# Kernel optimization log

Hardware: AMD Instinct MI355X
Metric: run time of the kernel (lower is better)

Reference implementation:

```python
import jax, jax.numpy as jnp
import numpy as np

B, T, F, H, C = 512, 512, 128, 32, 6

def setup_inputs() -> dict:
    key = jax.random.key(0)
    ks = jax.random.split(key, 6)
    x = jax.random.normal(ks[0], (B, T, F), jnp.float32)
    # random valid lengths; zero-padded tails get masked by Masking(mask_value=0.0)
    lengths = jax.random.randint(ks[1], (B,), T // 4, T + 1)
    tmask = (jnp.arange(T)[None, :] < lengths[:, None]).astype(jnp.float32)
    x = x * tmask[:, :, None]
    Wx = jax.random.normal(ks[2], (F, 4 * H), jnp.float32) / np.sqrt(F).astype(np.float32)
    Wh = jax.random.normal(ks[3], (H, 4 * H), jnp.float32) / np.sqrt(H).astype(np.float32)
    b = jnp.zeros((4 * H,), jnp.float32)
    Wfc = jax.random.normal(ks[4], (H, C), jnp.float32) / np.sqrt(H).astype(np.float32)
    bfc = jnp.zeros((C,), jnp.float32)
    return dict(x=x, Wx=Wx, Wh=Wh, b=b, Wfc=Wfc, bfc=bfc)

def reference(x, Wx, Wh, b, Wfc, bfc):
    # Masking(0.0): timestep masked iff all features == 0
    mask = jnp.any(x != 0.0, axis=-1)                       # [B, T]
    Hh = Wh.shape[0]
    Bn = x.shape[0]
    xt = jnp.transpose(x, (1, 0, 2))                        # [T, B, F]
    mt = jnp.transpose(mask, (1, 0))[:, :, None].astype(x.dtype)  # [T, B, 1]
    # precompute input projection for all steps (one big GEMM)
    xz = jnp.einsum('tbf,fk->tbk', xt, Wx) + b              # [T, B, 4H]

    def step(carry, inp):
        h, c = carry
        zx, m = inp
        z = zx + h @ Wh                                     # [B, 4H]
        i, f, g, o = jnp.split(z, 4, axis=-1)               # keras gate order i,f,c,o
        i = jax.nn.sigmoid(i)
        f = jax.nn.sigmoid(f)
        g = jnp.tanh(g)
        o = jax.nn.sigmoid(o)
        c_new = f * c + i * g
        h_new = o * jnp.tanh(c_new)
        # masked steps keep previous state (Keras masked LSTM semantics)
        h = m * h_new + (1.0 - m) * h
        c = m * c_new + (1.0 - m) * c
        return (h, c), None

    h0 = jnp.zeros((Bn, Hh), x.dtype)
    (h, _), _ = jax.lax.scan(step, (h0, h0), (xz, mt))
    return jax.nn.softmax(h @ Wfc + bfc, axis=-1)           # [B, C]
```

## Files before the change

kernel.cpp:

```cpp
#include <hip/hip_runtime.h>

#define B_ 512
#define T_ 512
#define F_ 128
#define H_ 32
#define C_ 6

__global__ __launch_bounds__(256, 2) void k_xz(
    const float* __restrict__ x, const float* __restrict__ W,
    const float* __restrict__ bias, float* __restrict__ xz,
    float* __restrict__ mask)
{
  __shared__ float xl[128 * 64];
  __shared__ float wl[64 * 128];
  const int tid = threadIdx.x;
  const int m0  = blockIdx.x * 128;
  const int cg  = tid & 15;
  const int rg  = tid >> 4;

  float4 xpre[8], wpre[8];
  int rowbits = 0;

  auto load_chunk = [&](int ch) {
#pragma unroll
    for (int k = 0; k < 8; ++k) {
      const int u = tid + k * 256, r = u >> 4, q = u & 15;
      xpre[k] = *(const float4*)(x + (size_t)(m0 + r) * 128 + ch * 64 + q * 4);
    }
#pragma unroll
    for (int k = 0; k < 8; ++k) {
      const int u = tid + k * 256, f = u >> 5, q = u & 31;
      wpre[k] = *(const float4*)(W + (size_t)(ch * 64 + f) * 128 + q * 4);
    }
  };
  auto mask_chunk = [&]() {
#pragma unroll
    for (int k = 0; k < 8; ++k) {
      const float4 v = xpre[k];
      int nb = ((v.x != 0.f) || (v.y != 0.f) || (v.z != 0.f) || (v.w != 0.f)) ? 1 : 0;
      nb |= __shfl_xor(nb, 1); nb |= __shfl_xor(nb, 2);
      nb |= __shfl_xor(nb, 4); nb |= __shfl_xor(nb, 8);
      rowbits |= nb << k;
    }
  };
  auto write_chunk = [&]() {
#pragma unroll
    for (int k = 0; k < 8; ++k) {
      const int u = tid + k * 256, r = u >> 4, q = u & 15;
      *(float4*)(xl + r * 64 + ((q * 4) ^ (((r >> 3) & 3) << 2))) = xpre[k];
    }
#pragma unroll
    for (int k = 0; k < 8; ++k) {
      const int u = tid + k * 256, f = u >> 5, q = u & 31;
      *(float4*)(wl + f * 128 + q * 4) = wpre[k];
    }
  };

  float acc[8][8];
#pragma unroll
  for (int r = 0; r < 8; ++r)
#pragma unroll
    for (int u = 0; u < 8; ++u) acc[r][u] = 0.f;

  auto compute = [&]() {
#pragma unroll 2
    for (int fq = 0; fq < 16; ++fq) {
      float4 xv[8];
#pragma unroll
      for (int r = 0; r < 8; ++r)
        xv[r] = *(const float4*)(xl + (rg * 8 + r) * 64 + ((fq * 4) ^ ((rg & 3) << 2)));
#pragma unroll
      for (int ff = 0; ff < 4; ++ff) {
        const float* wr = wl + (fq * 4 + ff) * 128 + cg * 4;
        const float4 wa = *(const float4*)(wr);
        const float4 wb = *(const float4*)(wr + 64);
#pragma unroll
        for (int r = 0; r < 8; ++r) {
          const float xs = (ff == 0) ? xv[r].x : (ff == 1) ? xv[r].y
                         : (ff == 2) ? xv[r].z : xv[r].w;
          acc[r][0] += xs * wa.x;  acc[r][1] += xs * wa.y;
          acc[r][2] += xs * wa.z;  acc[r][3] += xs * wa.w;
          acc[r][4] += xs * wb.x;  acc[r][5] += xs * wb.y;
          acc[r][6] += xs * wb.z;  acc[r][7] += xs * wb.w;
        }
      }
    }
  };

  load_chunk(0);
  mask_chunk();
  write_chunk();
  __syncthreads();
  load_chunk(1);
  compute();
  __syncthreads();
  mask_chunk();
  write_chunk();
  __syncthreads();
  compute();

  float bb[8];
#pragma unroll
  for (int u = 0; u < 4; ++u) {
    bb[u]     = bias[cg * 4 + u];
    bb[4 + u] = bias[64 + cg * 4 + u];
  }
#pragma unroll
  for (int r = 0; r < 8; ++r) {
    float* op = xz + (size_t)(m0 + rg * 8 + r) * 128;
    float4 o0 = { acc[r][0] + bb[0], acc[r][1] + bb[1], acc[r][2] + bb[2], acc[r][3] + bb[3] };
    float4 o1 = { acc[r][4] + bb[4], acc[r][5] + bb[5], acc[r][6] + bb[6], acc[r][7] + bb[7] };
    *(float4*)(op + cg * 4)      = o0;
    *(float4*)(op + 64 + cg * 4) = o1;
  }
  if ((tid & 15) == 0) {
#pragma unroll
    for (int k = 0; k < 8; ++k)
      mask[m0 + k * 16 + rg] = (rowbits >> k) & 1 ? 1.f : 0.f;
  }
}

__device__ __forceinline__ float sigmf(float xx) {
  return __builtin_amdgcn_rcpf(1.f + __expf(-xx));
}
__device__ __forceinline__ float tanhf_(float xx) {
  return __builtin_amdgcn_rcpf(1.f + __expf(-2.f * xx)) * 2.f - 1.f;
}

__global__ __launch_bounds__(64, 1) void k_lstm(
    const float* __restrict__ xz, const float* __restrict__ mask,
    const float* __restrict__ Wh, const float* __restrict__ Wfc,
    const float* __restrict__ bfc, float* __restrict__ out)
{
  const int lane = threadIdx.x;
  const int half = lane >> 5;
  const int j    = lane & 31;
  const int b    = blockIdx.x;

  const int colA = half * 32 + j;
  const int colB = 64 + half * 32 + j;

  float WhA[32], WhB[32];
#pragma unroll
  for (int f = 0; f < 32; ++f) {
    WhA[f] = Wh[f * 128 + colA];
    WhB[f] = Wh[f * 128 + colB];
  }

  float hsc[32];
#pragma unroll
  for (int f = 0; f < 32; ++f) hsc[f] = 0.f;

  float cj = 0.f, hj = 0.f;

  const float* xrow = xz + (size_t)b * (T_ * 128);
  const float* mp   = mask + (size_t)b * T_;

  float xa[4], xb[4], mr[4];
#pragma unroll
  for (int s = 0; s < 4; ++s) {
    xa[s] = xrow[s * 128 + colA];
    xb[s] = xrow[s * 128 + colB];
    mr[s] = mp[s];
  }

  for (int t0 = 0; t0 < T_; t0 += 4) {
#pragma unroll
    for (int s = 0; s < 4; ++s) {
      const int t = t0 + s;
      float zA0 = xa[s], zA1 = 0.f;
      float zB0 = xb[s], zB1 = 0.f;
      const float m = mr[s];

      int pf = t + 4;
      if (pf > T_ - 1) pf = T_ - 1;
      xa[s] = xrow[(size_t)pf * 128 + colA];
      xb[s] = xrow[(size_t)pf * 128 + colB];
      mr[s] = mp[pf];

#pragma unroll
      for (int f = 0; f < 16; ++f) {
        zA0 += hsc[2 * f]     * WhA[2 * f];
        zA1 += hsc[2 * f + 1] * WhA[2 * f + 1];
        zB0 += hsc[2 * f]     * WhB[2 * f];
        zB1 += hsc[2 * f + 1] * WhB[2 * f + 1];
      }
      const float zA = zA0 + zA1;
      const float zB = zB0 + zB1;
      const float oA = __shfl_xor(zA, 32);
      const float oB = __shfl_xor(zB, 32);
      const float zi = half ? oA : zA;
      const float zf = half ? zA : oA;
      const float zg = half ? oB : zB;
      const float zo = half ? zB : oB;

      const float ig = sigmf(zi);
      const float fg = sigmf(zf);
      const float gg = tanhf_(zg);
      const float og = sigmf(zo);
      const float cn = fg * cj + ig * gg;
      const float hn = og * tanhf_(cn);
      cj += m * (cn - cj);
      hj += m * (hn - hj);

#pragma unroll
      for (int f = 0; f < 32; ++f)
        hsc[f] = __uint_as_float(__builtin_amdgcn_readlane(__float_as_uint(hj), f));
    }
  }

  float logits[C_];
#pragma unroll
  for (int c = 0; c < C_; ++c) {
    float aa = bfc[c];
#pragma unroll
    for (int f = 0; f < 32; ++f) aa += hsc[f] * Wfc[f * C_ + c];
    logits[c] = aa;
  }
  if (lane == 0) {
    float mx = logits[0];
#pragma unroll
    for (int c = 1; c < C_; ++c) mx = fmaxf(mx, logits[c]);
    float e[C_], sden = 0.f;
#pragma unroll
    for (int c = 0; c < C_; ++c) { e[c] = __expf(logits[c] - mx); sden += e[c]; }
    const float rs = 1.f / sden;
#pragma unroll
    for (int c = 0; c < C_; ++c) out[(size_t)b * C_ + c] = e[c] * rs;
  }
}

extern "C" void kernel_launch(void* const* d_in, const int* in_sizes, int n_in,
                              void* d_out, int out_size, void* d_ws, size_t ws_size,
                              hipStream_t stream) {
  const float* x   = (const float*)d_in[0];
  const float* Wx  = (const float*)d_in[1];
  const float* Wh  = (const float*)d_in[2];
  const float* bv  = (const float*)d_in[3];
  const float* Wfc = (const float*)d_in[4];
  const float* bfc = (const float*)d_in[5];
  float* out = (float*)d_out;

  float* xz   = (float*)d_ws;
  float* mask = (float*)((char*)d_ws + (size_t)B_ * T_ * 128 * 4);

  k_xz<<<(B_ * T_) / 128, 256, 0, stream>>>(x, Wx, bv, xz, mask);
  k_lstm<<<B_, 64, 0, stream>>>(xz, mask, Wh, Wfc, bfc, out);
}
```

Baseline: 271.3 us.

## Fuse input projection into LSTM kernel with producer-consumer warp specialization

Replaces the separate input-projection GEMM kernel and recurrent kernel with one fused kernel. Per block, four producer waves compute the x@Wx projection chunk by chunk into a double-buffered shared-memory ring, and two consumer waves run the recurrence for two batch rows. This removes the round trip of the large xz intermediate through global memory and one launch. In exchange the projection runs as a per-timestep dot product with 128-register weights instead of a tiled GEMM, every chunk adds a block-wide barrier, and each block carries a large shared-memory footprint.

```diff
diff --git a/kernel.cpp b/kernel.cpp
--- a/kernel.cpp
+++ b/kernel.cpp
@@ -5,120 +5,9 @@
 #define F_ 128
 #define H_ 32
 #define C_ 6
-
-__global__ __launch_bounds__(256, 2) void k_xz(
-    const float* __restrict__ x, const float* __restrict__ W,
-    const float* __restrict__ bias, float* __restrict__ xz,
-    float* __restrict__ mask)
-{
-  __shared__ float xl[128 * 64];
-  __shared__ float wl[64 * 128];
-  const int tid = threadIdx.x;
-  const int m0  = blockIdx.x * 128;
-  const int cg  = tid & 15;
-  const int rg  = tid >> 4;
-
-  float4 xpre[8], wpre[8];
-  int rowbits = 0;
-
-  auto load_chunk = [&](int ch) {
-#pragma unroll
-    for (int k = 0; k < 8; ++k) {
-      const int u = tid + k * 256, r = u >> 4, q = u & 15;
-      xpre[k] = *(const float4*)(x + (size_t)(m0 + r) * 128 + ch * 64 + q * 4);
-    }
-#pragma unroll
-    for (int k = 0; k < 8; ++k) {
-      const int u = tid + k * 256, f = u >> 5, q = u & 31;
-      wpre[k] = *(const float4*)(W + (size_t)(ch * 64 + f) * 128 + q * 4);
-    }
-  };
-  auto mask_chunk = [&]() {
-#pragma unroll
-    for (int k = 0; k < 8; ++k) {
-      const float4 v = xpre[k];
-      int nb = ((v.x != 0.f) || (v.y != 0.f) || (v.z != 0.f) || (v.w != 0.f)) ? 1 : 0;
-      nb |= __shfl_xor(nb, 1); nb |= __shfl_xor(nb, 2);
-      nb |= __shfl_xor(nb, 4); nb |= __shfl_xor(nb, 8);
-      rowbits |= nb << k;
-    }
-  };
-  auto write_chunk = [&]() {
-#pragma unroll
-    for (int k = 0; k < 8; ++k) {
-      const int u = tid + k * 256, r = u >> 4, q = u & 15;
-      *(float4*)(xl + r * 64 + ((q * 4) ^ (((r >> 3) & 3) << 2))) = xpre[k];
-    }
-#pragma unroll
-    for (int k = 0; k < 8; ++k) {
-      const int u = tid + k * 256, f = u >> 5, q = u & 31;
-      *(float4*)(wl + f * 128 + q * 4) = wpre[k];
-    }
-  };
-
-  float acc[8][8];
-#pragma unroll
-  for (int r = 0; r < 8; ++r)
-#pragma unroll
-    for (int u = 0; u < 8; ++u) acc[r][u] = 0.f;
-
-  auto compute = [&]() {
-#pragma unroll 2
-    for (int fq = 0; fq < 16; ++fq) {
-      float4 xv[8];
-#pragma unroll
-      for (int r = 0; r < 8; ++r)
-        xv[r] = *(const float4*)(xl + (rg * 8 + r) * 64 + ((fq * 4) ^ ((rg & 3) << 2)));
-#pragma unroll
-      for (int ff = 0; ff < 4; ++ff) {
-        const float* wr = wl + (fq * 4 + ff) * 128 + cg * 4;
-        const float4 wa = *(const float4*)(wr);
-        const float4 wb = *(const float4*)(wr + 64);
-#pragma unroll
-        for (int r = 0; r < 8; ++r) {
-          const float xs = (ff == 0) ? xv[r].x : (ff == 1) ? xv[r].y
-                         : (ff == 2) ? xv[r].z : xv[r].w;
-          acc[r][0] += xs * wa.x;  acc[r][1] += xs * wa.y;
-          acc[r][2] += xs * wa.z;  acc[r][3] += xs * wa.w;
-          acc[r][4] += xs * wb.x;  acc[r][5] += xs * wb.y;
-          acc[r][6] += xs * wb.z;  acc[r][7] += xs * wb.w;
-        }
-      }
-    }
-  };
-
-  load_chunk(0);
-  mask_chunk();
-  write_chunk();
-  __syncthreads();
-  load_chunk(1);
-  compute();
-  __syncthreads();
-  mask_chunk();
-  write_chunk();
-  __syncthreads();
-  compute();
-
-  float bb[8];
-#pragma unroll
-  for (int u = 0; u < 4; ++u) {
-    bb[u]     = bias[cg * 4 + u];
-    bb[4 + u] = bias[64 + cg * 4 + u];
-  }
-#pragma unroll
-  for (int r = 0; r < 8; ++r) {
-    float* op = xz + (size_t)(m0 + rg * 8 + r) * 128;
-    float4 o0 = { acc[r][0] + bb[0], acc[r][1] + bb[1], acc[r][2] + bb[2], acc[r][3] + bb[3] };
-    float4 o1 = { acc[r][4] + bb[4], acc[r][5] + bb[5], acc[r][6] + bb[6], acc[r][7] + bb[7] };
-    *(float4*)(op + cg * 4)      = o0;
-    *(float4*)(op + 64 + cg * 4) = o1;
-  }
-  if ((tid & 15) == 0) {
-#pragma unroll
-    for (int k = 0; k < 8; ++k)
-      mask[m0 + k * 16 + rg] = (rowbits >> k) & 1 ? 1.f : 0.f;
-  }
-}
+#define CH 32
+#define NCH (T_ / CH)
+
 
 __device__ __forceinline__ float sigmf(float xx) {
   return __builtin_amdgcn_rcpf(1.f + __expf(-xx));
@@ -127,16 +16,89 @@
   return __builtin_amdgcn_rcpf(1.f + __expf(-2.f * xx)) * 2.f - 1.f;
 }
 
-__global__ __launch_bounds__(64, 1) void k_lstm(
-    const float* __restrict__ xz, const float* __restrict__ mask,
-    const float* __restrict__ Wh, const float* __restrict__ Wfc,
-    const float* __restrict__ bfc, float* __restrict__ out)
+__global__ __launch_bounds__(384, 2) void k_fused(
+    const float* __restrict__ x, const float* __restrict__ Wx,
+    const float* __restrict__ bias, const float* __restrict__ Wh,
+    const float* __restrict__ Wfc, const float* __restrict__ bfc,
+    float* __restrict__ out)
 {
-  const int lane = threadIdx.x;
+  __shared__ float zring[2][2][CH][128];
+  __shared__ float xst  [2][2][CH][128];
+  __shared__ float mring[2][NCH][CH];
+
+  const int tid  = threadIdx.x;
+  const int wid  = tid >> 6;
+  const int lane = tid & 63;
+  const int brow = blockIdx.x * 2;
+
+  if (wid >= 2) {
+    const int p    = wid - 2;
+    const int prow = p >> 1;
+    const int hp   = p & 1;
+    const int cb   = hp * 64;
+    const int sb   = hp * 16;
+    const int r    = brow + prow;
+
+    float Wc[128];
+#pragma unroll
+    for (int f = 0; f < 128; ++f) Wc[f] = Wx[f * 128 + cb + lane];
+    const float bb = bias[cb + lane];
+    const float* xr = x + (size_t)r * (T_ * F_);
+
+    float2 xld[16];
+#pragma unroll
+    for (int s = 0; s < 16; ++s)
+      xld[s] = *(const float2*)(xr + (sb + s) * F_ + 2 * lane);
+#pragma unroll
+    for (int s = 0; s < 16; ++s) {
+      *(float2*)(&xst[prow][0][sb + s][2 * lane]) = xld[s];
+      const bool nb = (xld[s].x != 0.f) || (xld[s].y != 0.f);
+      const unsigned long long bal = __ballot(nb);
+      if (lane == 0) mring[prow][0][sb + s] = bal ? 1.f : 0.f;
+    }
+
+    for (int ph = 0; ph <= NCH; ++ph) {
+      __syncthreads();
+      if (ph >= NCH) continue;
+      const int slot = ph & 1;
+
+      if (ph + 1 < NCH) {
+#pragma unroll
+        for (int s = 0; s < 16; ++s)
+          xld[s] = *(const float2*)(xr + ((ph + 1) * CH + sb + s) * F_ + 2 * lane);
+      }
+
+      for (int t = 0; t < CH; ++t) {
+        float z0 = bb, z1 = 0.f, z2 = 0.f, z3 = 0.f;
+        const float* xp = &xst[prow][slot][t][0];
+#pragma unroll
+        for (int fq = 0; fq < 32; ++fq) {
+          const float4 xf = *(const float4*)(xp + fq * 4);
+          z0 += xf.x * Wc[fq * 4 + 0];
+          z1 += xf.y * Wc[fq * 4 + 1];
+          z2 += xf.z * Wc[fq * 4 + 2];
+          z3 += xf.w * Wc[fq * 4 + 3];
+        }
+        zring[prow][slot][t][cb + lane] = (z0 + z1) + (z2 + z3);
+      }
+
+      if (ph + 1 < NCH) {
+#pragma unroll
+        for (int s = 0; s < 16; ++s) {
+          *(float2*)(&xst[prow][slot ^ 1][sb + s][2 * lane]) = xld[s];
+          const bool nb = (xld[s].x != 0.f) || (xld[s].y != 0.f);
+          const unsigned long long bal = __ballot(nb);
+          if (lane == 0) mring[prow][ph + 1][sb + s] = bal ? 1.f : 0.f;
+        }
+      }
+    }
+    return;
+  }
+
+  const int row  = wid;
+  const int r    = brow + row;
   const int half = lane >> 5;
   const int j    = lane & 31;
-  const int b    = blockIdx.x;
-
   const int colA = half * 32 + j;
   const int colB = 64 + half * 32 + j;
 
@@ -150,62 +112,64 @@
   float hsc[32];
 #pragma unroll
   for (int f = 0; f < 32; ++f) hsc[f] = 0.f;
-
   float cj = 0.f, hj = 0.f;
 
-  const float* xrow = xz + (size_t)b * (T_ * 128);
-  const float* mp   = mask + (size_t)b * T_;
-
-  float xa[4], xb[4], mr[4];
-#pragma unroll
-  for (int s = 0; s < 4; ++s) {
-    xa[s] = xrow[s * 128 + colA];
-    xb[s] = xrow[s * 128 + colB];
-    mr[s] = mp[s];
-  }
-
-  for (int t0 = 0; t0 < T_; t0 += 4) {
-#pragma unroll
-    for (int s = 0; s < 4; ++s) {
-      const int t = t0 + s;
-      float zA0 = xa[s], zA1 = 0.f;
-      float zB0 = xb[s], zB1 = 0.f;
-      const float m = mr[s];
-
-      int pf = t + 4;
-      if (pf > T_ - 1) pf = T_ - 1;
-      xa[s] = xrow[(size_t)pf * 128 + colA];
-      xb[s] = xrow[(size_t)pf * 128 + colB];
-      mr[s] = mp[pf];
-
-#pragma unroll
-      for (int f = 0; f < 16; ++f) {
-        zA0 += hsc[2 * f]     * WhA[2 * f];
-        zA1 += hsc[2 * f + 1] * WhA[2 * f + 1];
-        zB0 += hsc[2 * f]     * WhB[2 * f];
-        zB1 += hsc[2 * f + 1] * WhB[2 * f + 1];
-      }
-      const float zA = zA0 + zA1;
-      const float zB = zB0 + zB1;
-      const float oA = __shfl_xor(zA, 32);
-      const float oB = __shfl_xor(zB, 32);
-      const float zi = half ? oA : zA;
-      const float zf = half ? zA : oA;
-      const float zg = half ? oB : zB;
-      const float zo = half ? zB : oB;
-
-      const float ig = sigmf(zi);
-      const float fg = sigmf(zf);
-      const float gg = tanhf_(zg);
-      const float og = sigmf(zo);
-      const float cn = fg * cj + ig * gg;
-      const float hn = og * tanhf_(cn);
-      cj += m * (cn - cj);
-      hj += m * (hn - hj);
-
-#pragma unroll
-      for (int f = 0; f < 32; ++f)
-        hsc[f] = __uint_as_float(__builtin_amdgcn_readlane(__float_as_uint(hj), f));
+  for (int ph = 0; ph <= NCH; ++ph) {
+    __syncthreads();
+    if (ph < 1) continue;
+    const int c    = ph - 1;
+    const int slot = c & 1;
+    const float* zb = &zring[row][slot][0][0];
+    const float* mb = &mring[row][c][0];
+
+    float za[4], zc[4], mm[4];
+#pragma unroll
+    for (int u = 0; u < 4; ++u) {
+      za[u] = zb[u * 128 + colA];
+      zc[u] = zb[u * 128 + colB];
+      mm[u] = mb[u];
+    }
+    for (int s0 = 0; s0 < 8; ++s0) {
+#pragma unroll
+      for (int u = 0; u < 4; ++u) {
+        const int s = s0 * 4 + u;
+        float zA0 = za[u], zA1 = 0.f;
+        float zB0 = zc[u], zB1 = 0.f;
+        const float m = mm[u];
+        if (s0 < 7) {
+          za[u] = zb[(s + 4) * 128 + colA];
+          zc[u] = zb[(s + 4) * 128 + colB];
+          mm[u] = mb[s + 4];
+        }
+#pragma unroll
+        for (int f = 0; f < 16; ++f) {
+          zA0 += hsc[2 * f]     * WhA[2 * f];
+          zA1 += hsc[2 * f + 1] * WhA[2 * f + 1];
+          zB0 += hsc[2 * f]     * WhB[2 * f];
+          zB1 += hsc[2 * f + 1] * WhB[2 * f + 1];
+        }
+        const float zA = zA0 + zA1;
+        const float zB = zB0 + zB1;
+        const float oA = __shfl_xor(zA, 32);
+        const float oB = __shfl_xor(zB, 32);
+        const float zi = half ? oA : zA;
+        const float zf = half ? zA : oA;
+        const float zg = half ? oB : zB;
+        const float zo = half ? zB : oB;
+
+        const float ig = sigmf(zi);
+        const float fg = sigmf(zf);
+        const float gg = tanhf_(zg);
+        const float og = sigmf(zo);
+        const float cn = fg * cj + ig * gg;
+        const float hn = og * tanhf_(cn);
+        cj += m * (cn - cj);
+        hj += m * (hn - hj);
+
+#pragma unroll
+        for (int f = 0; f < 32; ++f)
+          hsc[f] = __uint_as_float(__builtin_amdgcn_readlane(__float_as_uint(hj), f));
+      }
     }
   }
 
@@ -226,7 +190,7 @@
     for (int c = 0; c < C_; ++c) { e[c] = __expf(logits[c] - mx); sden += e[c]; }
     const float rs = 1.f / sden;
 #pragma unroll
-    for (int c = 0; c < C_; ++c) out[(size_t)b * C_ + c] = e[c] * rs;
+    for (int c = 0; c < C_; ++c) out[(size_t)r * C_ + c] = e[c] * rs;
   }
 }
 
@@ -241,9 +205,5 @@
   const float* bfc = (const float*)d_in[5];
   float* out = (float*)d_out;
 
-  float* xz   = (float*)d_ws;
-  float* mask = (float*)((char*)d_ws + (size_t)B_ * T_ * 128 * 4);
-
-  k_xz<<<(B_ * T_) / 128, 256, 0, stream>>>(x, Wx, bv, xz, mask);
-  k_lstm<<<B_, 64, 0, stream>>>(xz, mask, Wh, Wfc, bfc, out);
-}
+  k_fused<<<B_ / 2, 384, 0, stream>>>(x, Wx, bv, Wh, Wfc, bfc, out);
+}
```

Result: slower. 904.7 us (+233.5%).

## Stage LSTM input projections through double-buffered LDS chunks in recurrent kernel

Applied to the files above, without the earlier changes.

The recurrent kernel now copies each 32-step chunk of the precomputed input projection from global memory into a double-buffered shared-memory tile. The next chunk is loaded with coalesced float4 reads spread across the inner steps, and the mask row is preloaded into LDS. This replaces per-step scattered global loads with LDS reads, aiming to take global latency off the serial dependency chain. The dot product is also split into four accumulators per gate to shorten the FMA chain, and the launch-bounds occupancy hint is dropped. The cost is higher register pressure from the float4 staging registers and about 33 KB of shared memory per block.

```diff
diff --git a/kernel.cpp b/kernel.cpp
--- a/kernel.cpp
+++ b/kernel.cpp
@@ -5,6 +5,8 @@
 #define F_ 128
 #define H_ 32
 #define C_ 6
+#define CH 32
+#define NCH (T_ / CH)
 
 __global__ __launch_bounds__(256, 2) void k_xz(
     const float* __restrict__ x, const float* __restrict__ W,
@@ -127,18 +129,31 @@
   return __builtin_amdgcn_rcpf(1.f + __expf(-2.f * xx)) * 2.f - 1.f;
 }
 
-__global__ __launch_bounds__(64, 1) void k_lstm(
+__global__ __launch_bounds__(64) void k_lstm(
     const float* __restrict__ xz, const float* __restrict__ mask,
     const float* __restrict__ Wh, const float* __restrict__ Wfc,
     const float* __restrict__ bfc, float* __restrict__ out)
 {
+  __shared__ float xch[2][CH][128];
+  __shared__ float mld[T_];
+
   const int lane = threadIdx.x;
   const int half = lane >> 5;
   const int j    = lane & 31;
   const int b    = blockIdx.x;
-
   const int colA = half * 32 + j;
   const int colB = 64 + half * 32 + j;
+
+  const float* xrow = xz + (size_t)b * (T_ * 128);
+  const float* mrow = mask + (size_t)b * T_;
+
+  {
+    float mv[8];
+#pragma unroll
+    for (int c = 0; c < 8; ++c) mv[c] = mrow[c * 64 + lane];
+#pragma unroll
+    for (int c = 0; c < 8; ++c) mld[c * 64 + lane] = mv[c];
+  }
 
   float WhA[32], WhB[32];
 #pragma unroll
@@ -147,65 +162,100 @@
     WhB[f] = Wh[f * 128 + colB];
   }
 
+  {
+    float4 xl[4];
+#pragma unroll
+    for (int g = 0; g < 4; ++g) {
+#pragma unroll
+      for (int u = 0; u < 4; ++u)
+        xl[u] = *(const float4*)(xrow + (g * 4 + u) * 256 + lane * 4);
+#pragma unroll
+      for (int u = 0; u < 4; ++u)
+        *(float4*)(&xch[0][0][0] + (g * 4 + u) * 256 + lane * 4) = xl[u];
+    }
+  }
+
   float hsc[32];
 #pragma unroll
   for (int f = 0; f < 32; ++f) hsc[f] = 0.f;
-
   float cj = 0.f, hj = 0.f;
 
-  const float* xrow = xz + (size_t)b * (T_ * 128);
-  const float* mp   = mask + (size_t)b * T_;
-
-  float xa[4], xb[4], mr[4];
-#pragma unroll
-  for (int s = 0; s < 4; ++s) {
-    xa[s] = xrow[s * 128 + colA];
-    xb[s] = xrow[s * 128 + colB];
-    mr[s] = mp[s];
-  }
-
-  for (int t0 = 0; t0 < T_; t0 += 4) {
-#pragma unroll
-    for (int s = 0; s < 4; ++s) {
-      const int t = t0 + s;
-      float zA0 = xa[s], zA1 = 0.f;
-      float zB0 = xb[s], zB1 = 0.f;
-      const float m = mr[s];
-
-      int pf = t + 4;
-      if (pf > T_ - 1) pf = T_ - 1;
-      xa[s] = xrow[(size_t)pf * 128 + colA];
-      xb[s] = xrow[(size_t)pf * 128 + colB];
-      mr[s] = mp[pf];
-
-#pragma unroll
-      for (int f = 0; f < 16; ++f) {
-        zA0 += hsc[2 * f]     * WhA[2 * f];
-        zA1 += hsc[2 * f + 1] * WhA[2 * f + 1];
-        zB0 += hsc[2 * f]     * WhB[2 * f];
-        zB1 += hsc[2 * f + 1] * WhB[2 * f + 1];
+  float4 stg[4];
+
+  for (int k = 0; k < NCH; ++k) {
+    const int slot = k & 1;
+    const float* zb = &xch[slot][0][0];
+    float* zn = &xch[slot ^ 1][0][0];
+    const float* mb = &mld[k * CH];
+    const float* xnext = xrow + (size_t)(k + 1) * (CH * 128);
+    const bool more = (k + 1 < NCH);
+
+    float za[4], zc[4], mm[4];
+#pragma unroll
+    for (int u = 0; u < 4; ++u) {
+      za[u] = zb[u * 128 + colA];
+      zc[u] = zb[u * 128 + colB];
+      mm[u] = mb[u];
+    }
+
+    for (int s0 = 0; s0 < 8; ++s0) {
+      if (more) {
+        const int g = s0 >> 1;
+        if ((s0 & 1) == 0) {
+#pragma unroll
+          for (int u = 0; u < 4; ++u)
+            stg[u] = *(const float4*)(xnext + (g * 4 + u) * 256 + lane * 4);
+        } else {
+#pragma unroll
+          for (int u = 0; u < 4; ++u)
+            *(float4*)(zn + (g * 4 + u) * 256 + lane * 4) = stg[u];
+        }
       }
-      const float zA = zA0 + zA1;
-      const float zB = zB0 + zB1;
-      const float oA = __shfl_xor(zA, 32);
-      const float oB = __shfl_xor(zB, 32);
-      const float zi = half ? oA : zA;
-      const float zf = half ? zA : oA;
-      const float zg = half ? oB : zB;
-      const float zo = half ? zB : oB;
-
-      const float ig = sigmf(zi);
-      const float fg = sigmf(zf);
-      const float gg = tanhf_(zg);
-      const float og = sigmf(zo);
-      const float cn = fg * cj + ig * gg;
-      const float hn = og * tanhf_(cn);
-      cj += m * (cn - cj);
-      hj += m * (hn - hj);
-
-#pragma unroll
-      for (int f = 0; f < 32; ++f)
-        hsc[f] = __uint_as_float(__builtin_amdgcn_readlane(__float_as_uint(hj), f));
+
+#pragma unroll
+      for (int u = 0; u < 4; ++u) {
+        const int s = s0 * 4 + u;
+        const float m = mm[u];
+        float a0 = za[u], a1 = 0.f, a2 = 0.f, a3 = 0.f;
+        float b0 = zc[u], b1 = 0.f, b2 = 0.f, b3 = 0.f;
+        if (s0 < 7) {
+          za[u] = zb[(s + 4) * 128 + colA];
+          zc[u] = zb[(s + 4) * 128 + colB];
+          mm[u] = mb[s + 4];
+        }
+#pragma unroll
+        for (int f = 0; f < 8; ++f) {
+          a0 += hsc[4 * f + 0] * WhA[4 * f + 0];
+          a1 += hsc[4 * f + 1] * WhA[4 * f + 1];
+          a2 += hsc[4 * f + 2] * WhA[4 * f + 2];
+          a3 += hsc[4 * f + 3] * WhA[4 * f + 3];
+          b0 += hsc[4 * f + 0] * WhB[4 * f + 0];
+          b1 += hsc[4 * f + 1] * WhB[4 * f + 1];
+          b2 += hsc[4 * f + 2] * WhB[4 * f + 2];
+          b3 += hsc[4 * f + 3] * WhB[4 * f + 3];
+        }
+        const float zA = (a0 + a1) + (a2 + a3);
+        const float zB = (b0 + b1) + (b2 + b3);
+        const float oA = __shfl_xor(zA, 32);
+        const float oB = __shfl_xor(zB, 32);
+        const float zi = half ? oA : zA;
+        const float zf = half ? zA : oA;
+        const float zg = half ? oB : zB;
+        const float zo = half ? zB : oB;
+
+        const float ig = sigmf(zi);
+        const float fg = sigmf(zf);
+        const float gg = tanhf_(zg);
+        const float og = sigmf(zo);
+        const float cn = fg * cj + ig * gg;
+        const float hn = og * tanhf_(cn);
+        cj += m * (cn - cj);
+        hj += m * (hn - hj);
+
+#pragma unroll
+        for (int f = 0; f < 32; ++f)
+          hsc[f] = __uint_as_float(__builtin_amdgcn_readlane(__float_as_uint(hj), f));
+      }
     }
   }
 
```

Result: slower. 318.4 us (+17.4%).
